# Kernel tuning notes

Measured on AMD Instinct MI355X. Metric: run time of the kernel, lower is better.

## Reference

```python
import jax, jax.numpy as jnp
import numpy as np

N = 50000       # nodes
E = 800000      # edges before self-loops (avg degree 16)
D_IN = 128
D_OUT = 128
DELTA = 2.5     # scaler normalization
EPS = 1e-5      # batchnorm eps
NEG_SLOPE = 0.01  # LeakyReLU default


def _lin_init(k, fan_in, shape):
    s = 1.0 / np.sqrt(fan_in)
    return jax.random.uniform(k, shape, jnp.float32, -s, s)


def setup_inputs() -> dict:
    key = jax.random.key(0)
    ks = jax.random.split(key, 12)
    ndata = jax.random.normal(ks[0], (N, D_IN), jnp.float32)
    src = jax.random.randint(ks[1], (E,), 0, N, jnp.int32)
    dst = jax.random.randint(ks[2], (E,), 0, N, jnp.int32)
    # PNAConvTower.M : Linear(2*in, in)
    M_w = _lin_init(ks[3], 2 * D_IN, (2 * D_IN, D_IN))
    M_b = _lin_init(ks[4], 2 * D_IN, (D_IN,))
    # PNAConvTower.U : Linear((3 aggs * 2 scalers + 1)*in, out) = Linear(7*in, out)
    U_w = _lin_init(ks[5], 7 * D_IN, (7 * D_IN, D_OUT))
    U_b = _lin_init(ks[6], 7 * D_IN, (D_OUT,))
    bn_gamma = jnp.ones((D_OUT,), jnp.float32)
    bn_beta = jnp.zeros((D_OUT,), jnp.float32)
    # PNAConv mixing layer: Linear(out, out) + LeakyReLU
    mix_w = _lin_init(ks[7], D_OUT, (D_OUT, D_OUT))
    mix_b = _lin_init(ks[8], D_OUT, (D_OUT,))
    return dict(ndata=ndata, M_w=M_w, M_b=M_b, U_w=U_w, U_b=U_b,
                bn_gamma=bn_gamma, bn_beta=bn_beta, mix_w=mix_w, mix_b=mix_b,
                src=src, dst=dst)


def reference(ndata, M_w, M_b, U_w, U_b, bn_gamma, bn_beta, mix_w, mix_b, src, dst):
    n = ndata.shape[0]
    # dgl.add_self_loop: append (i, i) for every node
    loop = jnp.arange(n, dtype=src.dtype)
    s = jnp.concatenate([src, loop])
    d = jnp.concatenate([dst, loop])
    # per-edge message: M(cat[h_src, h_dst])
    msg = jnp.concatenate([ndata[s], ndata[d]], axis=-1) @ M_w + M_b  # (E+N, D_IN)
    # in-degree per destination (>=1 due to self loops)
    deg = jax.ops.segment_sum(jnp.ones(d.shape, jnp.float32), d, num_segments=n)  # (N,)
    mean_agg = jax.ops.segment_sum(msg, d, num_segments=n) / deg[:, None]
    max_agg = jax.ops.segment_max(msg, d, num_segments=n)
    # aggregators ['mean','max','mean'] concatenated along feature dim
    agg = jnp.concatenate([mean_agg, max_agg, mean_agg], axis=-1)  # (N, 3*D_IN)
    # scalers ['identity','amplification'] applied to the concatenation
    amp = (jnp.log(deg + 1.0) / DELTA)[:, None]
    h_neigh = jnp.concatenate([agg, agg * amp], axis=-1)  # (N, 6*D_IN)
    # post-transform U on cat[node_feat, h_neigh]
    h = jnp.concatenate([ndata, h_neigh], axis=-1) @ U_w + U_b  # (N, D_OUT)
    # BatchNorm1d (training-mode batch stats, biased var)
    mu = h.mean(axis=0)
    var = ((h - mu) ** 2).mean(axis=0)
    h = (h - mu) * jax.lax.rsqrt(var + EPS) * bn_gamma + bn_beta
    # mixing layer: Linear + LeakyReLU
    out = h @ mix_w + mix_b
    return jax.nn.leaky_relu(out, NEG_SLOPE)
```

## Files before the change

### kernel.cpp

```cpp
#include <hip/hip_runtime.h>
#include <hip/hip_bf16.h>

#define NN 50000
#define EE 800000
#define DD 128
#define NT 3125
#define NBLK_SCAN 196

typedef short bf8 __attribute__((ext_vector_type(8)));
typedef float f32x4 __attribute__((ext_vector_type(4)));

__device__ __forceinline__ unsigned short f2b(float f) {
  __hip_bfloat16 h = __float2bfloat16(f);
  return *reinterpret_cast<unsigned short*>(&h);
}
__device__ __forceinline__ float b2f_bits(unsigned short s) {
  return __uint_as_float(((unsigned int)s) << 16);
}
__device__ __forceinline__ unsigned int pack2(float x, float y) {
  return (unsigned int)f2b(x) | ((unsigned int)f2b(y) << 16);
}

__global__ __launch_bounds__(256) void pack_all(
    const float* __restrict__ Mw, const float* __restrict__ Uw, const float* __restrict__ Mixw,
    unsigned short* __restrict__ Mp, unsigned short* __restrict__ Ui,
    unsigned short* __restrict__ Ua, unsigned short* __restrict__ Xx,
    unsigned int* __restrict__ cnt, float* __restrict__ bns, float* __restrict__ bnq) {
  int gid = blockIdx.x * 256 + threadIdx.x;
  if (gid < NN) cnt[gid] = 0u;
  if (gid < DD) { bns[gid] = 0.f; bnq[gid] = 0.f; }
  if (gid < 32768) {
    int g = gid;
    int j = g & 7, l = (g >> 3) & 63, ct = (g >> 9) & 15, kt = g >> 13;
    int k = kt * 32 + ((l >> 4) << 3) + j;
    int c = ct * 16 + (l & 15);
    float v = (c < 128) ? Mw[k * DD + c] : Mw[(128 + k) * DD + (c - 128)];
    Mp[g] = f2b(v);
  } else if (gid < 81920) {
    int g = gid - 32768;
    int j = g & 7, l = (g >> 3) & 63, ct = (g >> 9) & 7, kt = g >> 12;
    int k = kt * 32 + ((l >> 4) << 3) + j;
    int c = ct * 16 + (l & 15);
    float v = Uw[k * DD + c];
    if (k >= 128 && k < 256) v += Uw[(k + 256) * DD + c];
    Ui[g] = f2b(v);
  } else if (gid < 114688) {
    int g = gid - 81920;
    int j = g & 7, l = (g >> 3) & 63, ct = (g >> 9) & 7, kt = g >> 12;
    int k = kt * 32 + ((l >> 4) << 3) + j;
    int c = ct * 16 + (l & 15);
    float v = Uw[(512 + k) * DD + c];
    if (k < 128) v += Uw[(768 + k) * DD + c];
    Ua[g] = f2b(v);
  } else if (gid < 131072) {
    int g = gid - 114688;
    int j = g & 7, l = (g >> 3) & 63, ct = (g >> 9) & 7, kt = g >> 12;
    int k = kt * 32 + ((l >> 4) << 3) + j;
    int c = ct * 16 + (l & 15);
    Xx[g] = f2b(Mixw[k * DD + c]);
  }
}

__global__ __launch_bounds__(256) void pack_nd(
    const float* __restrict__ nd, unsigned int* __restrict__ ndp) {
  int gid = blockIdx.x * 256 + threadIdx.x;
  int n = gid >> 6, ln = gid & 63;
  float2 v = ((const float2*)nd)[gid];
  int uidx = (n >> 4) * 1024 + (ln >> 4) * 256 + (((ln >> 2) & 3) * 16 + (n & 15)) * 4 + (ln & 3);
  ndp[uidx] = pack2(v.x, v.y);
}

__global__ __launch_bounds__(256) void gemm_prep(
    const unsigned short* __restrict__ ndp, const unsigned short* __restrict__ Mp,
    const float* __restrict__ Mb, unsigned short* __restrict__ A16, float* __restrict__ Bv) {
  const int w = threadIdx.x >> 6, l = threadIdx.x & 63;
  const int half = w >> 1, strip = w & 1;
  const int row0 = blockIdx.x * 32 + strip * 16;
  const int tile = min(blockIdx.x * 2 + strip, NT - 1);
  const bf8* AP = (const bf8*)ndp;
  const bf8* B8 = (const bf8*)Mp;
  f32x4 zero = {0.f, 0.f, 0.f, 0.f};
  f32x4 acc[8];
  #pragma unroll
  for (int i = 0; i < 8; i++) acc[i] = zero;
  #pragma unroll
  for (int ks = 0; ks < 4; ks++) {
    bf8 a = AP[tile * 256 + ks * 64 + l];
    #pragma unroll
    for (int ct = 0; ct < 8; ct++) {
      bf8 b = B8[(ks * 16 + half * 8 + ct) * 64 + l];
      acc[ct] = __builtin_amdgcn_mfma_f32_16x16x32_bf16(a, b, acc[ct], 0, 0, 0);
    }
  }
  const int rb = row0 + (l >> 4) * 4;
  #pragma unroll
  for (int ct = 0; ct < 8; ct++) {
    int c = ct * 16 + (l & 15);
    float bias = half ? Mb[c] : 0.f;
    #pragma unroll
    for (int jj = 0; jj < 4; jj++) {
      int rr = rb + jj;
      if (rr < NN) {
        float v = acc[ct][jj] + bias;
        if (half) Bv[(size_t)rr * DD + c] = v;
        else      A16[(size_t)rr * DD + c] = f2b(v);
      }
    }
  }
}

__global__ __launch_bounds__(256) void deg_count(
    const int* __restrict__ dst, unsigned int* __restrict__ cnt) {
  int e = blockIdx.x * 256 + threadIdx.x;
  if (e < EE) atomicAdd(&cnt[dst[e]], 1u);
}

__global__ __launch_bounds__(256) void scan_blk(
    const unsigned int* __restrict__ cnt, unsigned int* __restrict__ loc,
    unsigned int* __restrict__ bsum) {
  __shared__ unsigned int sh[256];
  const int t = threadIdx.x;
  const int i = blockIdx.x * 256 + t;
  unsigned int v = (i < NN) ? cnt[i] : 0u;
  sh[t] = v;
  __syncthreads();
  for (int d = 1; d < 256; d <<= 1) {
    unsigned int u = (t >= d) ? sh[t - d] : 0u;
    __syncthreads();
    sh[t] += u;
    __syncthreads();
  }
  if (i < NN) loc[i] = sh[t] - v;
  if (t == 255) bsum[blockIdx.x] = sh[255];
}

__global__ __launch_bounds__(256) void scan_top(
    const unsigned int* __restrict__ bsum, unsigned int* __restrict__ bbase) {
  __shared__ unsigned int sh[256];
  const int t = threadIdx.x;
  unsigned int v = (t < NBLK_SCAN) ? bsum[t] : 0u;
  sh[t] = v;
  __syncthreads();
  for (int d = 1; d < 256; d <<= 1) {
    unsigned int u = (t >= d) ? sh[t - d] : 0u;
    __syncthreads();
    sh[t] += u;
    __syncthreads();
  }
  if (t < NBLK_SCAN) bbase[t] = sh[t] - v;
}

__global__ __launch_bounds__(256) void scan_fin(
    const unsigned int* __restrict__ loc, const unsigned int* __restrict__ bbase,
    unsigned int* __restrict__ off, unsigned int* __restrict__ cursor) {
  const int i = blockIdx.x * 256 + threadIdx.x;
  if (i < NN) {
    unsigned int o = loc[i] + bbase[blockIdx.x];
    off[i] = o; cursor[i] = o;
  }
  if (i == 0) off[NN] = EE;
}

__global__ __launch_bounds__(256) void fill_k(
    const int* __restrict__ src, const int* __restrict__ dst,
    unsigned int* __restrict__ cursor, unsigned int* __restrict__ eidx) {
  int e = blockIdx.x * 256 + threadIdx.x;
  if (e < EE) {
    unsigned int p = atomicAdd(&cursor[dst[e]], 1u);
    eidx[p] = (unsigned int)src[e];
  }
}

__global__ __launch_bounds__(256) void aggregate(
    const unsigned short* __restrict__ A16, const float* __restrict__ Bv,
    const unsigned int* __restrict__ off, const unsigned int* __restrict__ eidx,
    unsigned int* __restrict__ Sp, unsigned int* __restrict__ Xmp,
    float* __restrict__ amp) {
  int wave = threadIdx.x >> 6, ln = threadIdx.x & 63;
  int n = blockIdx.x * 4 + wave;
  if (n >= NN) return;
  const unsigned int* Au = (const unsigned int*)A16;
  unsigned int b0 = off[n], b1 = off[n + 1];
  unsigned int su = Au[(size_t)n * 64 + ln];
  float sx = b2f_bits((unsigned short)su), sy = b2f_bits((unsigned short)(su >> 16));
  float sumx = sx, sumy = sy, mxx = sx, mxy = sy;
  for (unsigned int j0 = b0; j0 < b1; j0 += 64) {
    int m = (int)min(64u, b1 - j0);
    int myi = (ln < m) ? (int)eidx[j0 + ln] : 0;
    for (int j = 0; j < m; j++) {
      int sN = __shfl(myi, j);
      unsigned int au = Au[(size_t)sN * 64 + ln];
      float ax = b2f_bits((unsigned short)au), ay = b2f_bits((unsigned short)(au >> 16));
      sumx += ax; sumy += ay;
      mxx = fmaxf(mxx, ax); mxy = fmaxf(mxy, ay);
    }
  }
  float degf = (float)(b1 - b0) + 1.f;
  float inv = 1.f / degf;
  float2 b = ((const float2*)(Bv + (size_t)n * DD))[ln];
  float smx = sumx * inv + b.x, smy = sumy * inv + b.y;
  float xmx = mxx + b.x, xmy = mxy + b.y;
  int uidx = (n >> 4) * 1024 + (ln >> 4) * 256 + (((ln >> 2) & 3) * 16 + (n & 15)) * 4 + (ln & 3);
  Sp[uidx] = pack2(smx, smy);
  Xmp[uidx] = pack2(xmx, xmy);
  if (ln == 0) amp[n] = logf(degf + 1.f) * 0.4f;
}

__global__ __launch_bounds__(256) void gemm_u(
    const unsigned short* __restrict__ ndp, const unsigned short* __restrict__ Sp,
    const unsigned short* __restrict__ Xmp, const float* __restrict__ amp,
    const unsigned short* __restrict__ Ui, const unsigned short* __restrict__ Ua,
    const float* __restrict__ Ub, unsigned short* __restrict__ Hp,
    float* __restrict__ bns, float* __restrict__ bnq) {
  const int w = threadIdx.x >> 6, l = threadIdx.x & 63;
  const int row0 = blockIdx.x * 64 + w * 16;
  const int tile = min(blockIdx.x * 4 + w, NT - 1);
  const bf8* ND = (const bf8*)ndp;
  const bf8* SS = (const bf8*)Sp;
  const bf8* XX = (const bf8*)Xmp;
  const bf8* BI = (const bf8*)Ui;
  const bf8* BA = (const bf8*)Ua;
  f32x4 zero = {0.f, 0.f, 0.f, 0.f};
  f32x4 accI[8], accA[8];
  #pragma unroll
  for (int i = 0; i < 8; i++) { accI[i] = zero; accA[i] = zero; }

  #pragma unroll
  for (int ks = 0; ks < 4; ks++) {
    bf8 a = ND[tile * 256 + ks * 64 + l];
    #pragma unroll
    for (int ct = 0; ct < 8; ct++)
      accI[ct] = __builtin_amdgcn_mfma_f32_16x16x32_bf16(a, BI[(ks * 8 + ct) * 64 + l], accI[ct], 0, 0, 0);
  }
  #pragma unroll
  for (int ks = 0; ks < 4; ks++) {
    bf8 a = SS[tile * 256 + ks * 64 + l];
    #pragma unroll
    for (int ct = 0; ct < 8; ct++)
      accI[ct] = __builtin_amdgcn_mfma_f32_16x16x32_bf16(a, BI[((4 + ks) * 8 + ct) * 64 + l], accI[ct], 0, 0, 0);
    #pragma unroll
    for (int ct = 0; ct < 8; ct++)
      accA[ct] = __builtin_amdgcn_mfma_f32_16x16x32_bf16(a, BA[(ks * 8 + ct) * 64 + l], accA[ct], 0, 0, 0);
  }
  #pragma unroll
  for (int ks = 0; ks < 4; ks++) {
    bf8 a = XX[tile * 256 + ks * 64 + l];
    #pragma unroll
    for (int ct = 0; ct < 8; ct++)
      accI[ct] = __builtin_amdgcn_mfma_f32_16x16x32_bf16(a, BI[((8 + ks) * 8 + ct) * 64 + l], accI[ct], 0, 0, 0);
    #pragma unroll
    for (int ct = 0; ct < 8; ct++)
      accA[ct] = __builtin_amdgcn_mfma_f32_16x16x32_bf16(a, BA[((4 + ks) * 8 + ct) * 64 + l], accA[ct], 0, 0, 0);
  }

  const int rb = row0 + (l >> 4) * 4;
  float ampv[4];
  #pragma unroll
  for (int jj = 0; jj < 4; jj++) ampv[jj] = amp[min(rb + jj, NN - 1)];

  #pragma unroll
  for (int ct = 0; ct < 8; ct++) {
    int c = ct * 16 + (l & 15);
    float ub = Ub[c];
    int hks = ct >> 1;
    int lpb = ((2 * ct + ((l >> 3) & 1)) & 3) * 16 + (l >> 4) * 4;
    int hj = l & 7;
    float sS = 0.f, sQ = 0.f;
    #pragma unroll
    for (int jj = 0; jj < 4; jj++) {
      int rr = rb + jj;
      if (rr < NN) {
        float h = accI[ct][jj] + ampv[jj] * accA[ct][jj] + ub;
        Hp[(size_t)tile * 2048 + hks * 512 + (lpb + jj) * 8 + hj] = f2b(h);
        sS += h; sQ += h * h;
      }
    }
    sS += __shfl_xor(sS, 16); sS += __shfl_xor(sS, 32);
    sQ += __shfl_xor(sQ, 16); sQ += __shfl_xor(sQ, 32);
    if ((l >> 4) == 0) {
      atomicAdd(bns + c, sS);
      atomicAdd(bnq + c, sQ);
    }
  }
}

__global__ __launch_bounds__(256) void gemm_final(
    const unsigned short* __restrict__ Hp, const float* __restrict__ bns,
    const float* __restrict__ bnq, const float* __restrict__ gamma,
    const float* __restrict__ beta, const unsigned short* __restrict__ Xx,
    const float* __restrict__ mixb, float* __restrict__ out) {
  const int w = threadIdx.x >> 6, l = threadIdx.x & 63;
  const int row0 = blockIdx.x * 64 + w * 16;
  const int tile = min(blockIdx.x * 4 + w, NT - 1);
  const bf8* HP = (const bf8*)Hp;
  const bf8* B8 = (const bf8*)Xx;
  const float invN = 1.f / (float)NN;
  f32x4 zero = {0.f, 0.f, 0.f, 0.f};
  f32x4 acc[8];
  #pragma unroll
  for (int i = 0; i < 8; i++) acc[i] = zero;

  #pragma unroll
  for (int ks = 0; ks < 4; ks++) {
    bf8 hp = HP[tile * 256 + ks * 64 + l];
    const int cb = ks * 32 + (l >> 4) * 8;
    bf8 a;
    #pragma unroll
    for (int j = 0; j < 8; j++) {
      int c = cb + j;
      float mu = bns[c] * invN;
      float var = bnq[c] * invN - mu * mu;
      float sc = gamma[c] * rsqrtf(var + 1e-5f);
      float ofs = beta[c] - mu * sc;
      float h = b2f_bits((unsigned short)hp[j]);
      a[j] = (short)f2b(fmaf(h, sc, ofs));
    }
    #pragma unroll
    for (int ct = 0; ct < 8; ct++)
      acc[ct] = __builtin_amdgcn_mfma_f32_16x16x32_bf16(a, B8[(ks * 8 + ct) * 64 + l], acc[ct], 0, 0, 0);
  }
  const int rb = row0 + (l >> 4) * 4;
  #pragma unroll
  for (int ct = 0; ct < 8; ct++) {
    int c = ct * 16 + (l & 15);
    float mbv = mixb[c];
    #pragma unroll
    for (int jj = 0; jj < 4; jj++) {
      int rr = rb + jj;
      if (rr < NN) {
        float o = acc[ct][jj] + mbv;
        o = o > 0.f ? o : 0.01f * o;
        out[(size_t)rr * DD + c] = o;
      }
    }
  }
}

extern "C" void kernel_launch(void* const* d_in, const int* in_sizes, int n_in,
                              void* d_out, int out_size, void* d_ws, size_t ws_size,
                              hipStream_t stream) {
  const float* nd    = (const float*)d_in[0];
  const float* Mw    = (const float*)d_in[1];
  const float* Mb    = (const float*)d_in[2];
  const float* Uw    = (const float*)d_in[3];
  const float* Ub    = (const float*)d_in[4];
  const float* gamma = (const float*)d_in[5];
  const float* beta  = (const float*)d_in[6];
  const float* mixw  = (const float*)d_in[7];
  const float* mixb  = (const float*)d_in[8];
  const int* src = (const int*)d_in[9];
  const int* dst = (const int*)d_in[10];
  float* out = (float*)d_out;

  float* ws  = (float*)d_ws;
  float* Bv  = ws;
  float* amp = Bv + (size_t)NN * DD;
  float* bns = amp + NN;
  float* bnq = bns + DD;
  unsigned short* A16 = (unsigned short*)(bnq + DD);
  unsigned short* ndp = A16 + (size_t)NN * DD;
  unsigned short* Sp  = ndp + (size_t)NT * 2048;
  unsigned short* Xmp = Sp + (size_t)NT * 2048;
  unsigned short* Hp  = Xmp + (size_t)NT * 2048;
  unsigned short* Mp  = Hp + (size_t)NT * 2048;
  unsigned short* Ui  = Mp + 32768;
  unsigned short* Ua  = Ui + 49152;
  unsigned short* Xx  = Ua + 32768;
  unsigned int* cnt    = (unsigned int*)(Xx + 16384);
  unsigned int* off    = cnt + NN;
  unsigned int* cursor = off + NN + 1;
  unsigned int* eidx   = cursor + NN;
  unsigned int* loc    = eidx + EE;
  unsigned int* bsum   = loc + NN;
  unsigned int* bbase  = bsum + 256;

  pack_all<<<512, 256, 0, stream>>>(Mw, Uw, mixw, Mp, Ui, Ua, Xx, cnt, bns, bnq);
  pack_nd<<<12500, 256, 0, stream>>>(nd, (unsigned int*)ndp);
  gemm_prep<<<(NN + 31) / 32, 256, 0, stream>>>(ndp, Mp, Mb, A16, Bv);
  deg_count<<<(EE + 255) / 256, 256, 0, stream>>>(dst, cnt);
  scan_blk<<<NBLK_SCAN, 256, 0, stream>>>(cnt, loc, bsum);
  scan_top<<<1, 256, 0, stream>>>(bsum, bbase);
  scan_fin<<<NBLK_SCAN, 256, 0, stream>>>(loc, bbase, off, cursor);
  fill_k<<<(EE + 255) / 256, 256, 0, stream>>>(src, dst, cursor, eidx);
  aggregate<<<(NN + 3) / 4, 256, 0, stream>>>(A16, Bv, off, eidx,
                                              (unsigned int*)Sp, (unsigned int*)Xmp, amp);
  gemm_u<<<(NN + 63) / 64, 256, 0, stream>>>(ndp, Sp, Xmp, amp, Ui, Ua, Ub, Hp, bns, bnq);
  gemm_final<<<(NN + 63) / 64, 256, 0, stream>>>(Hp, bns, bnq, gamma, beta, Xx, mixb, out);
}
```

Before: 435.6 us.

## Stage GEMM outputs through LDS for coalesced stores and batch gather loads

gemm_prep and gemm_u now write their bf16 results into shared memory first, then copy them out as coalesced 16-byte stores instead of scattered 2-byte global writes. The aggregate kernel unrolls its neighbor gather by 8 so several independent row loads are in flight before they are accumulated. gemm_u masks its out-of-range waves with a validity flag, and the Hp buffer is padded by three tiles. The cost is extra LDS use and a block barrier in each GEMM kernel.

```diff
diff --git a/kernel.cpp b/kernel.cpp
--- a/kernel.cpp
+++ b/kernel.cpp
@@ -73,6 +73,7 @@
 __global__ __launch_bounds__(256) void gemm_prep(
     const unsigned short* __restrict__ ndp, const unsigned short* __restrict__ Mp,
     const float* __restrict__ Mb, unsigned short* __restrict__ A16, float* __restrict__ Bv) {
+  __shared__ unsigned short alds[32 * DD];
   const int w = threadIdx.x >> 6, l = threadIdx.x & 63;
   const int half = w >> 1, strip = w & 1;
   const int row0 = blockIdx.x * 32 + strip * 16;
@@ -92,6 +93,7 @@
       acc[ct] = __builtin_amdgcn_mfma_f32_16x16x32_bf16(a, b, acc[ct], 0, 0, 0);
     }
   }
+  const int rl0 = strip * 16 + (l >> 4) * 4;
   const int rb = row0 + (l >> 4) * 4;
   #pragma unroll
   for (int ct = 0; ct < 8; ct++) {
@@ -103,9 +105,17 @@
       if (rr < NN) {
         float v = acc[ct][jj] + bias;
         if (half) Bv[(size_t)rr * DD + c] = v;
-        else      A16[(size_t)rr * DD + c] = f2b(v);
-      }
-    }
+        else      alds[(rl0 + jj) * DD + c] = f2b(v);
+      }
+    }
+  }
+  __syncthreads();
+  const uint4* ls = (const uint4*)alds;
+  uint4* gd = (uint4*)(A16 + (size_t)blockIdx.x * 32 * DD);
+  #pragma unroll
+  for (int e = threadIdx.x; e < 512; e += 256) {
+    int r = blockIdx.x * 32 + (e >> 4);
+    if (r < NN) gd[e] = ls[e];
   }
 }
 
@@ -187,8 +197,23 @@
   for (unsigned int j0 = b0; j0 < b1; j0 += 64) {
     int m = (int)min(64u, b1 - j0);
     int myi = (ln < m) ? (int)eidx[j0 + ln] : 0;
-    for (int j = 0; j < m; j++) {
-      int sN = __shfl(myi, j);
+    int jj = 0;
+    for (; jj + 8 <= m; jj += 8) {
+      unsigned int av[8];
+      #pragma unroll
+      for (int q = 0; q < 8; q++) {
+        int sN = __shfl(myi, jj + q);
+        av[q] = Au[(size_t)sN * 64 + ln];
+      }
+      #pragma unroll
+      for (int q = 0; q < 8; q++) {
+        float ax = b2f_bits((unsigned short)av[q]), ay = b2f_bits((unsigned short)(av[q] >> 16));
+        sumx += ax; sumy += ay;
+        mxx = fmaxf(mxx, ax); mxy = fmaxf(mxy, ay);
+      }
+    }
+    for (; jj < m; jj++) {
+      int sN = __shfl(myi, jj);
       unsigned int au = Au[(size_t)sN * 64 + ln];
       float ax = b2f_bits((unsigned short)au), ay = b2f_bits((unsigned short)(au >> 16));
       sumx += ax; sumy += ay;
@@ -212,9 +237,12 @@
     const unsigned short* __restrict__ Ui, const unsigned short* __restrict__ Ua,
     const float* __restrict__ Ub, unsigned short* __restrict__ Hp,
     float* __restrict__ bns, float* __restrict__ bnq) {
+  __shared__ unsigned short hlds[4 * 2048];
   const int w = threadIdx.x >> 6, l = threadIdx.x & 63;
   const int row0 = blockIdx.x * 64 + w * 16;
-  const int tile = min(blockIdx.x * 4 + w, NT - 1);
+  const int tileIdx = blockIdx.x * 4 + w;
+  const bool valid = tileIdx < NT;
+  const int tile = valid ? tileIdx : NT - 1;
   const bf8* ND = (const bf8*)ndp;
   const bf8* SS = (const bf8*)Sp;
   const bf8* XX = (const bf8*)Xmp;
@@ -258,30 +286,35 @@
   #pragma unroll
   for (int jj = 0; jj < 4; jj++) ampv[jj] = amp[min(rb + jj, NN - 1)];
 
-  #pragma unroll
-  for (int ct = 0; ct < 8; ct++) {
-    int c = ct * 16 + (l & 15);
-    float ub = Ub[c];
-    int hks = ct >> 1;
-    int lpb = ((2 * ct + ((l >> 3) & 1)) & 3) * 16 + (l >> 4) * 4;
-    int hj = l & 7;
-    float sS = 0.f, sQ = 0.f;
-    #pragma unroll
-    for (int jj = 0; jj < 4; jj++) {
-      int rr = rb + jj;
-      if (rr < NN) {
+  if (valid) {
+    #pragma unroll
+    for (int ct = 0; ct < 8; ct++) {
+      int c = ct * 16 + (l & 15);
+      float ub = Ub[c];
+      int hks = ct >> 1;
+      int lpb = ((2 * ct + ((l >> 3) & 1)) & 3) * 16 + (l >> 4) * 4;
+      int hj = l & 7;
+      float sS = 0.f, sQ = 0.f;
+      #pragma unroll
+      for (int jj = 0; jj < 4; jj++) {
         float h = accI[ct][jj] + ampv[jj] * accA[ct][jj] + ub;
-        Hp[(size_t)tile * 2048 + hks * 512 + (lpb + jj) * 8 + hj] = f2b(h);
+        hlds[w * 2048 + hks * 512 + (lpb + jj) * 8 + hj] = f2b(h);
         sS += h; sQ += h * h;
       }
-    }
-    sS += __shfl_xor(sS, 16); sS += __shfl_xor(sS, 32);
-    sQ += __shfl_xor(sQ, 16); sQ += __shfl_xor(sQ, 32);
-    if ((l >> 4) == 0) {
-      atomicAdd(bns + c, sS);
-      atomicAdd(bnq + c, sQ);
-    }
-  }
+      sS += __shfl_xor(sS, 16); sS += __shfl_xor(sS, 32);
+      sQ += __shfl_xor(sQ, 16); sQ += __shfl_xor(sQ, 32);
+      if ((l >> 4) == 0) {
+        atomicAdd(bns + c, sS);
+        atomicAdd(bnq + c, sQ);
+      }
+    }
+  }
+  __syncthreads();
+  int ntile = NT - blockIdx.x * 4;
+  if (ntile > 4) ntile = 4;
+  const uint4* ls = (const uint4*)hlds;
+  uint4* gd = (uint4*)(Hp + (size_t)blockIdx.x * 8192);
+  for (int e = threadIdx.x; e < ntile * 256; e += 256) gd[e] = ls[e];
 }
 
 __global__ __launch_bounds__(256) void gemm_final(
@@ -362,7 +395,7 @@
   unsigned short* Sp  = ndp + (size_t)NT * 2048;
   unsigned short* Xmp = Sp + (size_t)NT * 2048;
   unsigned short* Hp  = Xmp + (size_t)NT * 2048;
-  unsigned short* Mp  = Hp + (size_t)NT * 2048;
+  unsigned short* Mp  = Hp + (size_t)(NT + 3) * 2048;
   unsigned short* Ui  = Mp + 32768;
   unsigned short* Ua  = Ui + 49152;
   unsigned short* Xx  = Ua + 32768;
```

New measurement: 424.9 us. 2.4% less time.
